# Kernel optimization log

Hardware: AMD Instinct MI355X
Metric: run time of the kernel (lower is better)

Reference implementation:

```python
import jax, jax.numpy as jnp
import numpy as np

N_NODES = 100000
N_EDGES = 1600000
IN_DIM = 128
HEADS = 4
OUT_DIM = 32
NEG_SLOPE = 0.2  # PyG GATConv default negative_slope


def setup_inputs() -> dict:
    key = jax.random.key(0)
    k_x, k_e, k_w, k_as, k_ad = jax.random.split(key, 5)
    x = jax.random.normal(k_x, (N_NODES, IN_DIM), dtype=jnp.float32)
    edge_index = jax.random.randint(k_e, (2, N_EDGES), 0, N_NODES, dtype=jnp.int64)
    # Glorot-style init for learned parameters (GATConv lin + attention vectors)
    W = jax.random.normal(k_w, (IN_DIM, HEADS * OUT_DIM), dtype=jnp.float32) / np.sqrt(IN_DIM)
    att_src = jax.random.normal(k_as, (HEADS, OUT_DIM), dtype=jnp.float32) / np.sqrt(OUT_DIM)
    att_dst = jax.random.normal(k_ad, (HEADS, OUT_DIM), dtype=jnp.float32) / np.sqrt(OUT_DIM)
    bias = jnp.zeros((HEADS * OUT_DIM,), dtype=jnp.float32)
    return {"x": x, "edge_index": edge_index, "W": W, "att_src": att_src,
            "att_dst": att_dst, "bias": bias}


def reference(x, edge_index, W, att_src, att_dst, bias):
    N = x.shape[0]
    H, D = att_src.shape
    # PyG GATConv default: add self loops
    loop = jnp.arange(N, dtype=edge_index.dtype)
    src = jnp.concatenate([edge_index[0], loop])  # message sources  [E+N]
    dst = jnp.concatenate([edge_index[1], loop])  # message targets  [E+N]

    h = (x @ W).reshape(N, H, D)                          # [N, H, D]
    a_src = jnp.einsum('nhd,hd->nh', h, att_src)          # [N, H]
    a_dst = jnp.einsum('nhd,hd->nh', h, att_dst)          # [N, H]

    # per-edge attention logits, LeakyReLU(neg_slope=0.2)
    e = jax.nn.leaky_relu(a_src[src] + a_dst[dst], NEG_SLOPE)  # [E+N, H]

    # segment softmax over edges grouped by target node (numerically stable)
    e_max = jax.ops.segment_max(e, dst, num_segments=N)        # [N, H]
    e_max = jnp.where(jnp.isfinite(e_max), e_max, jnp.float32(0))
    ex = jnp.exp(e - e_max[dst])                               # [E+N, H]
    denom = jax.ops.segment_sum(ex, dst, num_segments=N)       # [N, H]
    alpha = ex / (denom[dst] + jnp.float32(1e-16))             # [E+N, H]

    # weighted scatter-aggregate of source features
    msg = h[src] * alpha[:, :, None]                           # [E+N, H, D]
    out = jax.ops.segment_sum(msg, dst, num_segments=N)        # [N, H, D]
    out = out.reshape(N, H * D) + bias                         # concat heads + bias
    return jax.nn.elu(out)                                     # wrapper ELU
```

## Files before the change

kernel.cpp:

```cpp
#include <hip/hip_runtime.h>
#include <hip/hip_fp16.h>
#include <math.h>

#define N_NODES 100000
#define N_EDGES 1600000
#define IN_DIM 128
#define F_DIM 128
#define NEG_SLOPE 0.2f

#define BUCKW_LOG 7
#define NBUCK 784
#define NBLK_S 100
#define EPSB 16000
#define SLAB_CAP 60
#define CSR_STRIDE 3072
#define GB 1563
#define PADBIT 0x80000000u

typedef short v8s __attribute__((ext_vector_type(8)));
typedef float v4f __attribute__((ext_vector_type(4)));

static __device__ __forceinline__ unsigned short f2bf(float f) {
    unsigned u = __float_as_uint(f);
    u += 0x7fffu + ((u >> 16) & 1u);
    return (unsigned short)(u >> 16);
}
static __device__ __forceinline__ float lo2f(unsigned u) { return __uint_as_float(u << 16); }
static __device__ __forceinline__ float hi2f(unsigned u) { return __uint_as_float(u & 0xffff0000u); }

__global__ __launch_bounds__(1024) void k_init(const float* __restrict__ W,
                                               unsigned short* __restrict__ Wt) {
    int i = blockIdx.x * 1024 + threadIdx.x;
    int n = i >> 7, k = i & 127;
    Wt[n * 128 + k] = f2bf(W[k * 128 + n]);
}

__global__ __launch_bounds__(256) void k_mega(const float* __restrict__ x,
                                              const unsigned short* __restrict__ Wt,
                                              unsigned short* __restrict__ h16,
                                              const float* __restrict__ att_src,
                                              const float* __restrict__ att_dst,
                                              float* __restrict__ a_src,
                                              float* __restrict__ a_dst,
                                              const int* __restrict__ ei,
                                              int* __restrict__ pcnt,
                                              int* __restrict__ ebuf) {
    __shared__ unsigned short As[64][136];
    __shared__ unsigned short Bs[128][136];
    __shared__ float attl[256];
    const int t = threadIdx.x;

    if (blockIdx.x >= GB) {
        int blk = blockIdx.x - GB;
        int* cur = (int*)&As[0][0];
        for (int i = t; i < NBUCK; i += 256) cur[i] = 0;
        __syncthreads();
        const int4* ps = (const int4*)(ei + blk * EPSB);
        const int4* pd = (const int4*)(ei + N_EDGES + blk * EPSB);
        for (int i = t; i < EPSB / 4; i += 256) {
            int4 s = ps[i];
            int4 d = pd[i];
            int b0 = d.x >> BUCKW_LOG; int r0 = atomicAdd(&cur[b0], 1);
            ebuf[(size_t)(b0 * NBLK_S + blk) * SLAB_CAP + r0] = s.x | ((d.x & 127) << 17);
            int b1 = d.y >> BUCKW_LOG; int r1 = atomicAdd(&cur[b1], 1);
            ebuf[(size_t)(b1 * NBLK_S + blk) * SLAB_CAP + r1] = s.y | ((d.y & 127) << 17);
            int b2 = d.z >> BUCKW_LOG; int r2 = atomicAdd(&cur[b2], 1);
            ebuf[(size_t)(b2 * NBLK_S + blk) * SLAB_CAP + r2] = s.z | ((d.z & 127) << 17);
            int b3 = d.w >> BUCKW_LOG; int r3 = atomicAdd(&cur[b3], 1);
            ebuf[(size_t)(b3 * NBLK_S + blk) * SLAB_CAP + r3] = s.w | ((d.w & 127) << 17);
        }
        __syncthreads();
        for (int b = t; b < NBUCK; b += 256) pcnt[b * NBLK_S + blk] = cur[b];
        return;
    }

    const int n0 = blockIdx.x * 64;
    attl[t] = (t < 128) ? att_src[t] : att_dst[t - 128];

    {
        int row = t >> 2, k0 = (t & 3) * 32;
        int n = n0 + row;
        #pragma unroll
        for (int i = 0; i < 4; i++) {
            float4 va = make_float4(0.f,0.f,0.f,0.f), vb = va;
            if (n < N_NODES) {
                const float* p = x + (size_t)n * IN_DIM + k0 + i * 8;
                va = *(const float4*)p;
                vb = *(const float4*)(p + 4);
            }
            uint4 u;
            u.x = f2bf(va.x) | ((unsigned)f2bf(va.y) << 16);
            u.y = f2bf(va.z) | ((unsigned)f2bf(va.w) << 16);
            u.z = f2bf(vb.x) | ((unsigned)f2bf(vb.y) << 16);
            u.w = f2bf(vb.z) | ((unsigned)f2bf(vb.w) << 16);
            *(uint4*)&As[row][k0 + i * 8] = u;
        }
    }
    {
        int nr = t >> 1, s0 = (t & 1) * 64;
        const uint4* src = (const uint4*)(Wt + nr * 128 + s0);
        #pragma unroll
        for (int i = 0; i < 8; i++)
            *(uint4*)&Bs[nr][s0 + i * 8] = src[i];
    }
    __syncthreads();

    const int w = t >> 6, lane = t & 63;
    const int mr = lane & 15, quad = lane >> 4;
    const int m0 = w * 16;

    v4f acc[8];
    #pragma unroll
    for (int nt = 0; nt < 8; nt++) acc[nt] = (v4f){0.f, 0.f, 0.f, 0.f};

    #pragma unroll
    for (int kk = 0; kk < 4; kk++) {
        int kof = kk * 32 + quad * 8;
        v8s a = *(const v8s*)&As[m0 + mr][kof];
        #pragma unroll
        for (int nt = 0; nt < 8; nt++) {
            v8s b = *(const v8s*)&Bs[nt * 16 + mr][kof];
            acc[nt] = __builtin_amdgcn_mfma_f32_16x16x32_bf16(a, b, acc[nt], 0, 0, 0);
        }
    }

    #pragma unroll
    for (int nt = 0; nt < 8; nt++)
        #pragma unroll
        for (int r = 0; r < 4; r++)
            As[m0 + quad * 4 + r][nt * 16 + mr] = f2bf(acc[nt][r]);
    __syncthreads();
    {
        int row = m0 + (lane >> 2);
        int c0  = (lane & 3) * 32;
        int n = n0 + row;
        if (n < N_NODES) {
            float ds = 0.f, dd = 0.f;
            #pragma unroll
            for (int i = 0; i < 4; i++) {
                uint4 v = *(const uint4*)&As[row][c0 + i * 8];
                *(uint4*)&h16[(size_t)n * F_DIM + c0 + i * 8] = v;
                float f0 = lo2f(v.x), f1 = hi2f(v.x);
                float f2 = lo2f(v.y), f3 = hi2f(v.y);
                float f4 = lo2f(v.z), f5 = hi2f(v.z);
                float f6 = lo2f(v.w), f7 = hi2f(v.w);
                const float* ps = &attl[c0 + i * 8];
                const float* pd = &attl[128 + c0 + i * 8];
                ds += f0*ps[0] + f1*ps[1] + f2*ps[2] + f3*ps[3]
                    + f4*ps[4] + f5*ps[5] + f6*ps[6] + f7*ps[7];
                dd += f0*pd[0] + f1*pd[1] + f2*pd[2] + f3*pd[3]
                    + f4*pd[4] + f5*pd[5] + f6*pd[6] + f7*pd[7];
            }
            int hd = lane & 3;
            a_src[n * 4 + hd] = ds;
            a_dst[n * 4 + hd] = dd;
        }
    }
}

__global__ __launch_bounds__(512) void k_csrfin(const int* __restrict__ ebuf,
                                                const int* __restrict__ pcnt,
                                                int2* __restrict__ ebounds,
                                                int* __restrict__ csr2) {
    __shared__ int cnt[128];
    __shared__ int off[128];
    __shared__ int scnt[NBLK_S];
    __shared__ int wtot;
    int b = blockIdx.x, tid = threadIdx.x;
    if (tid < NBLK_S) scnt[tid] = pcnt[b * NBLK_S + tid];
    if (tid < 128) cnt[tid] = 0;
    __syncthreads();
    int s = tid >> 2, i0 = tid & 3;
    const int* sb = ebuf + (size_t)(b * NBLK_S + s) * SLAB_CAP;
    int c = (s < NBLK_S) ? scnt[s] : 0;
    {
        int i = i0;
        for (; i + 4 < c; i += 8) {
            int e0 = sb[i];
            int e1 = sb[i + 4];
            atomicAdd(&cnt[(e0 >> 17) & 127], 1);
            atomicAdd(&cnt[(e1 >> 17) & 127], 1);
        }
        if (i < c) atomicAdd(&cnt[(sb[i] >> 17) & 127], 1);
    }
    __syncthreads();
    if (tid < 128) {
        int cp = (cnt[tid] + 3) & ~3;
        int x = cp;
        #pragma unroll
        for (int o = 1; o < 64; o <<= 1) {
            int y = __shfl_up(x, o, 64);
            if ((tid & 63) >= o) x += y;
        }
        off[tid] = x - cp;
        if (tid == 63) wtot = x;
    }
    __syncthreads();
    if (tid < 128) {
        int v = off[tid] + ((tid >= 64) ? wtot : 0) + b * CSR_STRIDE;
        off[tid] = v;
        int node = (b << BUCKW_LOG) + tid;
        int cc = cnt[tid];
        if (node < N_NODES) {
            ebounds[node] = make_int2(v, v + cc);
            int cpad = (cc + 3) & ~3;
            for (int k = cc; k < cpad; k++)
                csr2[v + k] = node | PADBIT;
        }
        cnt[tid] = 0;
    }
    __syncthreads();
    {
        int i = i0;
        for (; i + 4 < c; i += 8) {
            int e0 = sb[i];
            int e1 = sb[i + 4];
            int d0 = (e0 >> 17) & 127; int r0 = atomicAdd(&cnt[d0], 1);
            csr2[off[d0] + r0] = e0 & 0x1ffff;
            int d1 = (e1 >> 17) & 127; int r1 = atomicAdd(&cnt[d1], 1);
            csr2[off[d1] + r1] = e1 & 0x1ffff;
        }
        if (i < c) {
            int e0 = sb[i];
            int d0 = (e0 >> 17) & 127; int r0 = atomicAdd(&cnt[d0], 1);
            csr2[off[d0] + r0] = e0 & 0x1ffff;
        }
    }
}

__global__ __launch_bounds__(256) void k_agg(const uint4* __restrict__ h16x4,
                                             const float* __restrict__ a_src,
                                             const float* __restrict__ a_dst,
                                             const int2* __restrict__ ebounds,
                                             const int* __restrict__ csr2,
                                             const float* __restrict__ bias,
                                             float* __restrict__ out) {
    int n = (blockIdx.x * 256 + threadIdx.x) >> 6;
    if (n >= N_NODES) return;
    int lane = threadIdx.x & 63;
    int grp = lane >> 4, g = lane & 15, hd = g >> 2;

    float adn = a_dst[n * 4 + hd];
    float p0 = 0.f;
    if (grp == 0) {
        float e0 = a_src[n * 4 + hd] + adn;
        e0 = e0 > 0.f ? e0 : NEG_SLOPE * e0;
        p0 = __expf(e0);
    }
    uint4 hs = h16x4[(size_t)n * 16 + g];
    float l  = p0;
    float a0 = p0 * lo2f(hs.x), a1 = p0 * hi2f(hs.x);
    float a2 = p0 * lo2f(hs.y), a3 = p0 * hi2f(hs.y);
    float a4 = p0 * lo2f(hs.z), a5 = p0 * hi2f(hs.z);
    float a6 = p0 * lo2f(hs.w), a7 = p0 * hi2f(hs.w);

    int2 eb = ebounds[n];
    int beg = eb.x, cnt = eb.y - eb.x;
    const int* sp = csr2 + beg + grp;
    int steps = (cnt + 3) >> 2;
    int u0 = (steps > 0) ? sp[0] : 0;
    int u1 = (steps > 1) ? sp[4] : 0;
    int t = 0;
    for (; t + 2 <= steps; t += 2) {
        int s0 = u0 & 0x7fffffff;
        int s1 = u1 & 0x7fffffff;
        int m0 = u0, m1 = u1;
        float as0 = a_src[s0 * 4 + hd];
        float as1 = a_src[s1 * 4 + hd];
        uint4 h0 = h16x4[(size_t)s0 * 16 + g];
        uint4 h1 = h16x4[(size_t)s1 * 16 + g];
        int tn = t + 2;
        u0 = (tn < steps) ? sp[4 * tn] : 0;
        u1 = (tn + 1 < steps) ? sp[4 * tn + 4] : 0;
        float w0 = as0 + adn; w0 = w0 > 0.f ? w0 : NEG_SLOPE * w0;
        float w1 = as1 + adn; w1 = w1 > 0.f ? w1 : NEG_SLOPE * w1;
        float q0 = __expf(w0);
        float q1 = __expf(w1);
        q0 = m0 < 0 ? 0.f : q0;
        q1 = m1 < 0 ? 0.f : q1;
        l  += q0 + q1;
        a0 += q0 * lo2f(h0.x) + q1 * lo2f(h1.x);
        a1 += q0 * hi2f(h0.x) + q1 * hi2f(h1.x);
        a2 += q0 * lo2f(h0.y) + q1 * lo2f(h1.y);
        a3 += q0 * hi2f(h0.y) + q1 * hi2f(h1.y);
        a4 += q0 * lo2f(h0.z) + q1 * lo2f(h1.z);
        a5 += q0 * hi2f(h0.z) + q1 * hi2f(h1.z);
        a6 += q0 * lo2f(h0.w) + q1 * lo2f(h1.w);
        a7 += q0 * hi2f(h0.w) + q1 * hi2f(h1.w);
    }
    if (t < steps) {
        int s0 = u0 & 0x7fffffff;
        int m0 = u0;
        float as0 = a_src[s0 * 4 + hd];
        uint4 h0 = h16x4[(size_t)s0 * 16 + g];
        float w0 = as0 + adn; w0 = w0 > 0.f ? w0 : NEG_SLOPE * w0;
        float q0 = __expf(w0);
        q0 = m0 < 0 ? 0.f : q0;
        l  += q0;
        a0 += q0 * lo2f(h0.x);
        a1 += q0 * hi2f(h0.x);
        a2 += q0 * lo2f(h0.y);
        a3 += q0 * hi2f(h0.y);
        a4 += q0 * lo2f(h0.z);
        a5 += q0 * hi2f(h0.z);
        a6 += q0 * lo2f(h0.w);
        a7 += q0 * hi2f(h0.w);
    }
    #define RED2(v) v += __shfl_xor(v, 16, 64); v += __shfl_xor(v, 32, 64);
    RED2(l); RED2(a0); RED2(a1); RED2(a2); RED2(a3);
    RED2(a4); RED2(a5); RED2(a6); RED2(a7);
    #undef RED2

    if (grp == 0) {
        float inv = 1.f / (l + 1e-16f);
        float4 b0 = *(const float4*)&bias[g * 8];
        float4 b1 = *(const float4*)&bias[g * 8 + 4];
        float o0 = a0 * inv + b0.x, o1 = a1 * inv + b0.y;
        float o2 = a2 * inv + b0.z, o3 = a3 * inv + b0.w;
        float o4 = a4 * inv + b1.x, o5 = a5 * inv + b1.y;
        float o6 = a6 * inv + b1.z, o7 = a7 * inv + b1.w;
        o0 = o0 > 0.f ? o0 : __expf(o0) - 1.f;
        o1 = o1 > 0.f ? o1 : __expf(o1) - 1.f;
        o2 = o2 > 0.f ? o2 : __expf(o2) - 1.f;
        o3 = o3 > 0.f ? o3 : __expf(o3) - 1.f;
        o4 = o4 > 0.f ? o4 : __expf(o4) - 1.f;
        o5 = o5 > 0.f ? o5 : __expf(o5) - 1.f;
        o6 = o6 > 0.f ? o6 : __expf(o6) - 1.f;
        o7 = o7 > 0.f ? o7 : __expf(o7) - 1.f;
        *(float4*)&out[(size_t)n * F_DIM + g * 8]     = make_float4(o0, o1, o2, o3);
        *(float4*)&out[(size_t)n * F_DIM + g * 8 + 4] = make_float4(o4, o5, o6, o7);
    }
}

extern "C" void kernel_launch(void* const* d_in, const int* in_sizes, int n_in,
                              void* d_out, int out_size, void* d_ws, size_t ws_size,
                              hipStream_t stream) {
    const float* x       = (const float*)d_in[0];
    const int*   ei      = (const int*)d_in[1];
    const float* W       = (const float*)d_in[2];
    const float* att_src = (const float*)d_in[3];
    const float* att_dst = (const float*)d_in[4];
    const float* bias    = (const float*)d_in[5];
    float*       out     = (float*)d_out;

    char* ws = (char*)d_ws;
    unsigned short* h16 = (unsigned short*)ws; ws += (size_t)N_NODES * F_DIM * 2;
    unsigned short* Wt  = (unsigned short*)ws; ws += (size_t)IN_DIM * F_DIM * 2;
    float* a_src  = (float*)ws; ws += (size_t)N_NODES * 4 * 4;
    float* a_dst  = (float*)ws; ws += (size_t)N_NODES * 4 * 4;
    int*   pcnt   = (int*)ws;   ws += (size_t)NBUCK * NBLK_S * 4;
    int2*  ebounds= (int2*)ws;  ws += (size_t)N_NODES * 8 + 512;
    int*   ebuf   = (int*)ws;   ws += (size_t)NBUCK * NBLK_S * SLAB_CAP * 4;
    int*   csr2   = (int*)ws;   ws += (size_t)NBUCK * CSR_STRIDE * 4;

    k_init<<<16, 1024, 0, stream>>>(W, Wt);
    k_mega<<<GB + NBLK_S, 256, 0, stream>>>(x, Wt, h16, att_src, att_dst,
                                            a_src, a_dst, ei, pcnt, ebuf);
    k_csrfin<<<NBUCK, 512, 0, stream>>>(ebuf, pcnt, ebounds, csr2);
    k_agg<<<(N_NODES * 64 + 255) / 256, 256, 0, stream>>>((const uint4*)h16, a_src, a_dst, ebounds, csr2, bias, out);
}
```

Before: 262.1 us.

## Fuse CSR finalization into aggregation kernel using per-bucket shared-memory edge lists

Removes the separate CSR build kernel. Each aggregation block loads its bucket's edge slabs into a shared-memory per-node list of capacity 64 and aggregates its 128 nodes directly, with each wave processing 8 nodes serially. This eliminates the global csr2/ebounds write and reread and one kernel launch. In exchange, per-node degree is capped at 64, the grid drops to 784 large blocks with reduced latency hiding, and partitioning blocks are reordered to run first in k_mega.

```diff
diff --git a/kernel.cpp b/kernel.cpp
--- a/kernel.cpp
+++ b/kernel.cpp
@@ -12,8 +12,8 @@
 #define NBUCK 784
 #define NBLK_S 100
 #define EPSB 16000
-#define SLAB_CAP 60
-#define CSR_STRIDE 3072
+#define SLAB_CAP 64
+#define DEG_CAP 64
 #define GB 1563
 #define PADBIT 0x80000000u
 
@@ -50,8 +50,8 @@
     __shared__ float attl[256];
     const int t = threadIdx.x;
 
-    if (blockIdx.x >= GB) {
-        int blk = blockIdx.x - GB;
+    if (blockIdx.x < NBLK_S) {
+        int blk = blockIdx.x;
         int* cur = (int*)&As[0][0];
         for (int i = t; i < NBUCK; i += 256) cur[i] = 0;
         __syncthreads();
@@ -61,20 +61,20 @@
             int4 s = ps[i];
             int4 d = pd[i];
             int b0 = d.x >> BUCKW_LOG; int r0 = atomicAdd(&cur[b0], 1);
-            ebuf[(size_t)(b0 * NBLK_S + blk) * SLAB_CAP + r0] = s.x | ((d.x & 127) << 17);
+            ebuf[((b0 * NBLK_S + blk) << 6) + r0] = s.x | ((d.x & 127) << 17);
             int b1 = d.y >> BUCKW_LOG; int r1 = atomicAdd(&cur[b1], 1);
-            ebuf[(size_t)(b1 * NBLK_S + blk) * SLAB_CAP + r1] = s.y | ((d.y & 127) << 17);
+            ebuf[((b1 * NBLK_S + blk) << 6) + r1] = s.y | ((d.y & 127) << 17);
             int b2 = d.z >> BUCKW_LOG; int r2 = atomicAdd(&cur[b2], 1);
-            ebuf[(size_t)(b2 * NBLK_S + blk) * SLAB_CAP + r2] = s.z | ((d.z & 127) << 17);
+            ebuf[((b2 * NBLK_S + blk) << 6) + r2] = s.z | ((d.z & 127) << 17);
             int b3 = d.w >> BUCKW_LOG; int r3 = atomicAdd(&cur[b3], 1);
-            ebuf[(size_t)(b3 * NBLK_S + blk) * SLAB_CAP + r3] = s.w | ((d.w & 127) << 17);
+            ebuf[((b3 * NBLK_S + blk) << 6) + r3] = s.w | ((d.w & 127) << 17);
         }
         __syncthreads();
         for (int b = t; b < NBUCK; b += 256) pcnt[b * NBLK_S + blk] = cur[b];
         return;
     }
 
-    const int n0 = blockIdx.x * 64;
+    const int n0 = (blockIdx.x - NBLK_S) * 64;
     attl[t] = (t < 128) ? att_src[t] : att_dst[t - 128];
 
     {
@@ -158,177 +158,143 @@
     }
 }
 
-__global__ __launch_bounds__(512) void k_csrfin(const int* __restrict__ ebuf,
-                                                const int* __restrict__ pcnt,
-                                                int2* __restrict__ ebounds,
-                                                int* __restrict__ csr2) {
+__global__ __launch_bounds__(1024) void k_agg2(const uint4* __restrict__ h16x4,
+                                               const float* __restrict__ a_src,
+                                               const float* __restrict__ a_dst,
+                                               const int* __restrict__ pcnt,
+                                               const int* __restrict__ ebuf,
+                                               const float* __restrict__ bias,
+                                               float* __restrict__ out) {
+    __shared__ int list[128 << 6];
     __shared__ int cnt[128];
-    __shared__ int off[128];
     __shared__ int scnt[NBLK_S];
-    __shared__ int wtot;
-    int b = blockIdx.x, tid = threadIdx.x;
-    if (tid < NBLK_S) scnt[tid] = pcnt[b * NBLK_S + tid];
-    if (tid < 128) cnt[tid] = 0;
-    __syncthreads();
-    int s = tid >> 2, i0 = tid & 3;
-    const int* sb = ebuf + (size_t)(b * NBLK_S + s) * SLAB_CAP;
-    int c = (s < NBLK_S) ? scnt[s] : 0;
+    const int b = blockIdx.x, t = threadIdx.x;
+
+    if (t < NBLK_S) scnt[t] = pcnt[b * NBLK_S + t];
+    if (t < 128) cnt[t] = 0;
+    __syncthreads();
     {
-        int i = i0;
-        for (; i + 4 < c; i += 8) {
-            int e0 = sb[i];
-            int e1 = sb[i + 4];
-            atomicAdd(&cnt[(e0 >> 17) & 127], 1);
-            atomicAdd(&cnt[(e1 >> 17) & 127], 1);
-        }
-        if (i < c) atomicAdd(&cnt[(sb[i] >> 17) & 127], 1);
-    }
-    __syncthreads();
-    if (tid < 128) {
-        int cp = (cnt[tid] + 3) & ~3;
-        int x = cp;
-        #pragma unroll
-        for (int o = 1; o < 64; o <<= 1) {
-            int y = __shfl_up(x, o, 64);
-            if ((tid & 63) >= o) x += y;
-        }
-        off[tid] = x - cp;
-        if (tid == 63) wtot = x;
-    }
-    __syncthreads();
-    if (tid < 128) {
-        int v = off[tid] + ((tid >= 64) ? wtot : 0) + b * CSR_STRIDE;
-        off[tid] = v;
-        int node = (b << BUCKW_LOG) + tid;
-        int cc = cnt[tid];
-        if (node < N_NODES) {
-            ebounds[node] = make_int2(v, v + cc);
-            int cpad = (cc + 3) & ~3;
-            for (int k = cc; k < cpad; k++)
-                csr2[v + k] = node | PADBIT;
-        }
-        cnt[tid] = 0;
-    }
-    __syncthreads();
-    {
-        int i = i0;
-        for (; i + 4 < c; i += 8) {
-            int e0 = sb[i];
-            int e1 = sb[i + 4];
-            int d0 = (e0 >> 17) & 127; int r0 = atomicAdd(&cnt[d0], 1);
-            csr2[off[d0] + r0] = e0 & 0x1ffff;
-            int d1 = (e1 >> 17) & 127; int r1 = atomicAdd(&cnt[d1], 1);
-            csr2[off[d1] + r1] = e1 & 0x1ffff;
-        }
-        if (i < c) {
-            int e0 = sb[i];
-            int d0 = (e0 >> 17) & 127; int r0 = atomicAdd(&cnt[d0], 1);
-            csr2[off[d0] + r0] = e0 & 0x1ffff;
-        }
-    }
-}
-
-__global__ __launch_bounds__(256) void k_agg(const uint4* __restrict__ h16x4,
-                                             const float* __restrict__ a_src,
-                                             const float* __restrict__ a_dst,
-                                             const int2* __restrict__ ebounds,
-                                             const int* __restrict__ csr2,
-                                             const float* __restrict__ bias,
-                                             float* __restrict__ out) {
-    int n = (blockIdx.x * 256 + threadIdx.x) >> 6;
-    if (n >= N_NODES) return;
-    int lane = threadIdx.x & 63;
-    int grp = lane >> 4, g = lane & 15, hd = g >> 2;
-
-    float adn = a_dst[n * 4 + hd];
-    float p0 = 0.f;
-    if (grp == 0) {
-        float e0 = a_src[n * 4 + hd] + adn;
-        e0 = e0 > 0.f ? e0 : NEG_SLOPE * e0;
-        p0 = __expf(e0);
-    }
-    uint4 hs = h16x4[(size_t)n * 16 + g];
-    float l  = p0;
-    float a0 = p0 * lo2f(hs.x), a1 = p0 * hi2f(hs.x);
-    float a2 = p0 * lo2f(hs.y), a3 = p0 * hi2f(hs.y);
-    float a4 = p0 * lo2f(hs.z), a5 = p0 * hi2f(hs.z);
-    float a6 = p0 * lo2f(hs.w), a7 = p0 * hi2f(hs.w);
-
-    int2 eb = ebounds[n];
-    int beg = eb.x, cnt = eb.y - eb.x;
-    const int* sp = csr2 + beg + grp;
-    int steps = (cnt + 3) >> 2;
-    int u0 = (steps > 0) ? sp[0] : 0;
-    int u1 = (steps > 1) ? sp[4] : 0;
-    int t = 0;
-    for (; t + 2 <= steps; t += 2) {
-        int s0 = u0 & 0x7fffffff;
-        int s1 = u1 & 0x7fffffff;
-        int m0 = u0, m1 = u1;
-        float as0 = a_src[s0 * 4 + hd];
-        float as1 = a_src[s1 * 4 + hd];
-        uint4 h0 = h16x4[(size_t)s0 * 16 + g];
-        uint4 h1 = h16x4[(size_t)s1 * 16 + g];
-        int tn = t + 2;
-        u0 = (tn < steps) ? sp[4 * tn] : 0;
-        u1 = (tn + 1 < steps) ? sp[4 * tn + 4] : 0;
-        float w0 = as0 + adn; w0 = w0 > 0.f ? w0 : NEG_SLOPE * w0;
-        float w1 = as1 + adn; w1 = w1 > 0.f ? w1 : NEG_SLOPE * w1;
-        float q0 = __expf(w0);
-        float q1 = __expf(w1);
-        q0 = m0 < 0 ? 0.f : q0;
-        q1 = m1 < 0 ? 0.f : q1;
-        l  += q0 + q1;
-        a0 += q0 * lo2f(h0.x) + q1 * lo2f(h1.x);
-        a1 += q0 * hi2f(h0.x) + q1 * hi2f(h1.x);
-        a2 += q0 * lo2f(h0.y) + q1 * lo2f(h1.y);
-        a3 += q0 * hi2f(h0.y) + q1 * hi2f(h1.y);
-        a4 += q0 * lo2f(h0.z) + q1 * lo2f(h1.z);
-        a5 += q0 * hi2f(h0.z) + q1 * hi2f(h1.z);
-        a6 += q0 * lo2f(h0.w) + q1 * lo2f(h1.w);
-        a7 += q0 * hi2f(h0.w) + q1 * hi2f(h1.w);
-    }
-    if (t < steps) {
-        int s0 = u0 & 0x7fffffff;
-        int m0 = u0;
-        float as0 = a_src[s0 * 4 + hd];
-        uint4 h0 = h16x4[(size_t)s0 * 16 + g];
-        float w0 = as0 + adn; w0 = w0 > 0.f ? w0 : NEG_SLOPE * w0;
-        float q0 = __expf(w0);
-        q0 = m0 < 0 ? 0.f : q0;
-        l  += q0;
-        a0 += q0 * lo2f(h0.x);
-        a1 += q0 * hi2f(h0.x);
-        a2 += q0 * lo2f(h0.y);
-        a3 += q0 * hi2f(h0.y);
-        a4 += q0 * lo2f(h0.z);
-        a5 += q0 * hi2f(h0.z);
-        a6 += q0 * lo2f(h0.w);
-        a7 += q0 * hi2f(h0.w);
-    }
-    #define RED2(v) v += __shfl_xor(v, 16, 64); v += __shfl_xor(v, 32, 64);
-    RED2(l); RED2(a0); RED2(a1); RED2(a2); RED2(a3);
-    RED2(a4); RED2(a5); RED2(a6); RED2(a7);
-    #undef RED2
-
-    if (grp == 0) {
-        float inv = 1.f / (l + 1e-16f);
-        float4 b0 = *(const float4*)&bias[g * 8];
-        float4 b1 = *(const float4*)&bias[g * 8 + 4];
-        float o0 = a0 * inv + b0.x, o1 = a1 * inv + b0.y;
-        float o2 = a2 * inv + b0.z, o3 = a3 * inv + b0.w;
-        float o4 = a4 * inv + b1.x, o5 = a5 * inv + b1.y;
-        float o6 = a6 * inv + b1.z, o7 = a7 * inv + b1.w;
-        o0 = o0 > 0.f ? o0 : __expf(o0) - 1.f;
-        o1 = o1 > 0.f ? o1 : __expf(o1) - 1.f;
-        o2 = o2 > 0.f ? o2 : __expf(o2) - 1.f;
-        o3 = o3 > 0.f ? o3 : __expf(o3) - 1.f;
-        o4 = o4 > 0.f ? o4 : __expf(o4) - 1.f;
-        o5 = o5 > 0.f ? o5 : __expf(o5) - 1.f;
-        o6 = o6 > 0.f ? o6 : __expf(o6) - 1.f;
-        o7 = o7 > 0.f ? o7 : __expf(o7) - 1.f;
-        *(float4*)&out[(size_t)n * F_DIM + g * 8]     = make_float4(o0, o1, o2, o3);
-        *(float4*)&out[(size_t)n * F_DIM + g * 8 + 4] = make_float4(o4, o5, o6, o7);
+        const int4* win = (const int4*)(ebuf + (size_t)b * (NBLK_S * SLAB_CAP));
+        #pragma unroll
+        for (int it = 0; it < 2; it++) {
+            int i4 = it * 1024 + t;
+            if (i4 < NBLK_S * SLAB_CAP / 4) {
+                int4 e4 = win[i4];
+                int base = i4 << 2;
+                int es0 = e4.x, es1 = e4.y, es2 = e4.z, es3 = e4.w;
+                #define PUT(J, E) {                                            \
+                    int idx = base + (J);                                      \
+                    if ((idx & 63) < scnt[idx >> 6]) {                         \
+                        int dl = ((E) >> 17) & 127;                            \
+                        int r = atomicAdd(&cnt[dl], 1);                        \
+                        list[(dl << 6) + r] = (E) & 0x1ffff;                   \
+                    }                                                          \
+                }
+                PUT(0, es0); PUT(1, es1); PUT(2, es2); PUT(3, es3);
+                #undef PUT
+            }
+        }
+    }
+    __syncthreads();
+    if (t < 128) {
+        int c = cnt[t], cp = (c + 3) & ~3;
+        for (int k = c; k < cp; k++) list[(t << 6) + k] = (int)PADBIT;
+    }
+    __syncthreads();
+
+    const int wv = t >> 6, lane = t & 63;
+    const int grp = lane >> 4, g = lane & 15, hd = g >> 2;
+    const float4 bb0 = *(const float4*)&bias[g * 8];
+    const float4 bb1 = *(const float4*)&bias[g * 8 + 4];
+
+    for (int k8 = 0; k8 < 8; k8++) {
+        int nl = (wv << 3) + k8;
+        int n = (b << BUCKW_LOG) + nl;
+        if (n >= N_NODES) break;
+
+        float adn = a_dst[n * 4 + hd];
+        float p0 = 0.f;
+        if (grp == 0) {
+            float e0 = a_src[n * 4 + hd] + adn;
+            e0 = e0 > 0.f ? e0 : NEG_SLOPE * e0;
+            p0 = __expf(e0);
+        }
+        uint4 hs = h16x4[(size_t)n * 16 + g];
+        float l  = p0;
+        float a0 = p0 * lo2f(hs.x), a1 = p0 * hi2f(hs.x);
+        float a2 = p0 * lo2f(hs.y), a3 = p0 * hi2f(hs.y);
+        float a4 = p0 * lo2f(hs.z), a5 = p0 * hi2f(hs.z);
+        float a6 = p0 * lo2f(hs.w), a7 = p0 * hi2f(hs.w);
+
+        int cn = cnt[nl];
+        const int* sp = &list[(nl << 6) + grp];
+        int steps = (cn + 3) >> 2;
+        int tt = 0;
+        for (; tt + 2 <= steps; tt += 2) {
+            int u0 = sp[4 * tt];
+            int u1 = sp[4 * tt + 4];
+            int s0 = u0 & 0x7fffffff;
+            int s1 = u1 & 0x7fffffff;
+            float as0 = a_src[s0 * 4 + hd];
+            float as1 = a_src[s1 * 4 + hd];
+            uint4 h0 = h16x4[(size_t)s0 * 16 + g];
+            uint4 h1 = h16x4[(size_t)s1 * 16 + g];
+            float w0 = as0 + adn; w0 = w0 > 0.f ? w0 : NEG_SLOPE * w0;
+            float w1 = as1 + adn; w1 = w1 > 0.f ? w1 : NEG_SLOPE * w1;
+            float q0 = __expf(w0);
+            float q1 = __expf(w1);
+            q0 = u0 < 0 ? 0.f : q0;
+            q1 = u1 < 0 ? 0.f : q1;
+            l  += q0 + q1;
+            a0 += q0 * lo2f(h0.x) + q1 * lo2f(h1.x);
+            a1 += q0 * hi2f(h0.x) + q1 * hi2f(h1.x);
+            a2 += q0 * lo2f(h0.y) + q1 * lo2f(h1.y);
+            a3 += q0 * hi2f(h0.y) + q1 * hi2f(h1.y);
+            a4 += q0 * lo2f(h0.z) + q1 * lo2f(h1.z);
+            a5 += q0 * hi2f(h0.z) + q1 * hi2f(h1.z);
+            a6 += q0 * lo2f(h0.w) + q1 * lo2f(h1.w);
+            a7 += q0 * hi2f(h0.w) + q1 * hi2f(h1.w);
+        }
+        if (tt < steps) {
+            int u0 = sp[4 * tt];
+            int s0 = u0 & 0x7fffffff;
+            float as0 = a_src[s0 * 4 + hd];
+            uint4 h0 = h16x4[(size_t)s0 * 16 + g];
+            float w0 = as0 + adn; w0 = w0 > 0.f ? w0 : NEG_SLOPE * w0;
+            float q0 = __expf(w0);
+            q0 = u0 < 0 ? 0.f : q0;
+            l  += q0;
+            a0 += q0 * lo2f(h0.x);
+            a1 += q0 * hi2f(h0.x);
+            a2 += q0 * lo2f(h0.y);
+            a3 += q0 * hi2f(h0.y);
+            a4 += q0 * lo2f(h0.z);
+            a5 += q0 * hi2f(h0.z);
+            a6 += q0 * lo2f(h0.w);
+            a7 += q0 * hi2f(h0.w);
+        }
+        #define RED2(v) v += __shfl_xor(v, 16, 64); v += __shfl_xor(v, 32, 64);
+        RED2(l); RED2(a0); RED2(a1); RED2(a2); RED2(a3);
+        RED2(a4); RED2(a5); RED2(a6); RED2(a7);
+        #undef RED2
+
+        if (grp == 0) {
+            float inv = 1.f / (l + 1e-16f);
+            float o0 = a0 * inv + bb0.x, o1 = a1 * inv + bb0.y;
+            float o2 = a2 * inv + bb0.z, o3 = a3 * inv + bb0.w;
+            float o4 = a4 * inv + bb1.x, o5 = a5 * inv + bb1.y;
+            float o6 = a6 * inv + bb1.z, o7 = a7 * inv + bb1.w;
+            o0 = o0 > 0.f ? o0 : __expf(o0) - 1.f;
+            o1 = o1 > 0.f ? o1 : __expf(o1) - 1.f;
+            o2 = o2 > 0.f ? o2 : __expf(o2) - 1.f;
+            o3 = o3 > 0.f ? o3 : __expf(o3) - 1.f;
+            o4 = o4 > 0.f ? o4 : __expf(o4) - 1.f;
+            o5 = o5 > 0.f ? o5 : __expf(o5) - 1.f;
+            o6 = o6 > 0.f ? o6 : __expf(o6) - 1.f;
+            o7 = o7 > 0.f ? o7 : __expf(o7) - 1.f;
+            *(float4*)&out[(size_t)n * F_DIM + g * 8]     = make_float4(o0, o1, o2, o3);
+            *(float4*)&out[(size_t)n * F_DIM + g * 8 + 4] = make_float4(o4, o5, o6, o7);
+        }
     }
 }
 
@@ -349,13 +315,11 @@
     float* a_src  = (float*)ws; ws += (size_t)N_NODES * 4 * 4;
     float* a_dst  = (float*)ws; ws += (size_t)N_NODES * 4 * 4;
     int*   pcnt   = (int*)ws;   ws += (size_t)NBUCK * NBLK_S * 4;
-    int2*  ebounds= (int2*)ws;  ws += (size_t)N_NODES * 8 + 512;
     int*   ebuf   = (int*)ws;   ws += (size_t)NBUCK * NBLK_S * SLAB_CAP * 4;
-    int*   csr2   = (int*)ws;   ws += (size_t)NBUCK * CSR_STRIDE * 4;
 
     k_init<<<16, 1024, 0, stream>>>(W, Wt);
     k_mega<<<GB + NBLK_S, 256, 0, stream>>>(x, Wt, h16, att_src, att_dst,
                                             a_src, a_dst, ei, pcnt, ebuf);
-    k_csrfin<<<NBUCK, 512, 0, stream>>>(ebuf, pcnt, ebounds, csr2);
-    k_agg<<<(N_NODES * 64 + 255) / 256, 256, 0, stream>>>((const uint4*)h16, a_src, a_dst, ebounds, csr2, bias, out);
-}
+    k_agg2<<<NBUCK, 1024, 0, stream>>>((const uint4*)h16, a_src, a_dst,
+                                       pcnt, ebuf, bias, out);
+}
```

After: 242.2 us. 1.08x faster.
